# Kernel tuning notes

Hardware: AMD Instinct MI355X
Metric: run time of the kernel (lower is better)

## Reference

```python
import jax, jax.numpy as jnp
import numpy as np

DEGREE = 3
S_PNTS = 8          # sampling_points along polynomial
NUM_POINTS = 2      # deformable offsets per sampling point
S_SCALE = 0.077
SPATIAL = [(80, 80), (40, 40), (20, 20), (10, 10)]  # (h, w) per level
STARTS = [0, 6400, 8000, 8400]


def _lambdas():
    lam = jnp.linspace(0.0, 1.0, S_PNTS, dtype=jnp.float32)
    return jnp.stack([lam ** i for i in range(DEGREE, -1, -1)], 1)  # (S, degree+1)


def grid_sample_bilinear(img, grid):
    """torch F.grid_sample(mode=bilinear, padding_mode=zeros, align_corners=False).
    img: (B, C, H, W); grid: (B, Q, S, 2) with (x, y) in [-1, 1]. Returns (B, Q, S, C)."""
    B, C, H, W = img.shape
    gx = (grid[..., 0] + 1.0) * 0.5 * W - 0.5
    gy = (grid[..., 1] + 1.0) * 0.5 * H - 0.5
    x0 = jnp.floor(gx); y0 = jnp.floor(gy)
    x1 = x0 + 1.0;      y1 = y0 + 1.0
    wx1 = gx - x0; wx0 = 1.0 - wx1
    wy1 = gy - y0; wy0 = 1.0 - wy1
    flat = img.transpose(0, 2, 3, 1).reshape(B, H * W, C)  # (B, HW, C)
    Q, S = grid.shape[1], grid.shape[2]

    def fetch(xi, yi):
        valid = (xi >= 0) & (xi <= W - 1) & (yi >= 0) & (yi <= H - 1)
        xc = jnp.clip(xi, 0, W - 1).astype(jnp.int32)
        yc = jnp.clip(yi, 0, H - 1).astype(jnp.int32)
        idx = (yc * W + xc).reshape(B, Q * S, 1)
        vals = jnp.take_along_axis(flat, idx, axis=1).reshape(B, Q, S, C)
        return vals * valid[..., None].astype(img.dtype)

    out = (wy0 * wx0)[..., None] * fetch(x0, y0) \
        + (wy0 * wx1)[..., None] * fetch(x1, y0) \
        + (wy1 * wx0)[..., None] * fetch(x0, y1) \
        + (wy1 * wx1)[..., None] * fetch(x1, y1)
    return out  # (B, Q, S, C)


def setup_inputs() -> dict:
    key = jax.random.key(0)
    ks = jax.random.split(key, 6)
    B, Q, C = 8, 500, 256
    ref_polys = jax.random.uniform(ks[0], (B, Q, 2 * (DEGREE + 1)), dtype=jnp.float32)
    ref_levels = jax.random.randint(ks[1], (B, Q), 0, len(SPATIAL), dtype=jnp.int32)
    memory = jax.random.normal(ks[2], (B, 8500, C), dtype=jnp.float32)
    W1 = jax.random.normal(ks[3], (C, C), dtype=jnp.float32) * (1.0 / np.sqrt(C))
    b1 = jnp.zeros((C,), jnp.float32)
    W2 = jax.random.normal(ks[4], (C, 2 * NUM_POINTS), dtype=jnp.float32) * (1.0 / np.sqrt(C))
    b2 = jnp.zeros((2 * NUM_POINTS,), jnp.float32)
    return {"ref_polys": ref_polys, "ref_levels": ref_levels, "memory": memory,
            "W1": W1, "b1": b1, "W2": W2, "b2": b2}


def reference(ref_polys, ref_levels, memory, W1, b1, W2, b2):
    B, Q, _ = ref_polys.shape
    C = memory.shape[-1]
    lambdas = _lambdas()  # (S, degree+1)
    # polynomial evaluation: (B,Q,2,deg+1) @ (deg+1,S) -> (B,Q,S,2), mapped to [-1,1]
    rp = jax.lax.stop_gradient(ref_polys).reshape(B, Q, 2, DEGREE + 1)
    sampling_pts = 2.0 * (jnp.einsum('bqcd,sd->bqsc', rp, lambdas) - 0.5)  # (B,Q,S,2)
    # per-level bilinear sampling; memory slices reshaped to (B,C,h,w)
    sampled = []
    for (h, w), st in zip(SPATIAL, STARTS):
        lvl = memory[:, st:st + h * w, :].transpose(0, 2, 1).reshape(B, C, h, w)
        sampled.append(grid_sample_bilinear(lvl, sampling_pts))
    sampled = jnp.stack(sampled, 1)  # (B, L, Q, S, C)
    # gather the level assigned to each query
    idx = jnp.broadcast_to(ref_levels[:, None, :, None, None].astype(jnp.int32),
                           (B, 1, Q, S_PNTS, C))
    emb = jnp.take_along_axis(sampled, idx, axis=1)[:, 0]  # (B, Q, S, C)
    # 2-layer tanh MLP offset head
    h = jnp.tanh(emb @ W1 + b1)
    off = h @ W2 + b2  # (B, Q, S, 2*NUM_POINTS)
    off = S_SCALE * jnp.tanh(off.reshape(B, Q, S_PNTS, NUM_POINTS, 2))
    ref_points = off + sampling_pts[:, :, :, None, :]  # (B,Q,S,NP,2)
    return ref_points.reshape(B, Q, S_PNTS * NUM_POINTS, 2)
```

## Files before the change

kernel.cpp:

```cpp
#include <hip/hip_runtime.h>
#include <math.h>

#define S_PNTS 8
#define NUM_POINTS 2
#define NB 8
#define NQ 500
#define NC 256
#define S_SCALE 0.077f
#define QPB 8
#define ROWS (QPB * S_PNTS)
#define APAD 264

typedef __bf16 bf16x8 __attribute__((ext_vector_type(8)));
typedef __bf16 bf16x4 __attribute__((ext_vector_type(4)));
typedef float  f32x4  __attribute__((ext_vector_type(4)));

__device__ __forceinline__ float fast_tanh(float x) {
    float xc = fminf(fmaxf(x, -14.0f), 14.0f);
    float t  = __builtin_amdgcn_exp2f(xc * 2.88539008178f);
    return 1.0f - 2.0f * __builtin_amdgcn_rcpf(t + 1.0f);
}

__global__ __launch_bounds__(256) void prep_w1(const float* __restrict__ W1,
                                               __bf16* __restrict__ W1t) {
    __shared__ float tile[16][17];
    const int n0 = blockIdx.x * 16, k0 = blockIdx.y * 16;
    const int tx = threadIdx.x & 15, ty = threadIdx.x >> 4;
    tile[ty][tx] = W1[(k0 + ty) * NC + n0 + tx];
    __syncthreads();
    W1t[(n0 + ty) * NC + k0 + tx] = (__bf16)tile[tx][ty];
}

__global__ __launch_bounds__(256) void decoder_kernel(
    const float* __restrict__ ref_polys,
    const int*   __restrict__ ref_levels,
    const float* __restrict__ memory,
    const __bf16* __restrict__ W1t,
    const float* __restrict__ b1,
    const float* __restrict__ W2,
    const float* __restrict__ b2,
    float*       __restrict__ out)
{
    const int tid = threadIdx.x;

    __shared__ __bf16 emb_lds[ROWS * APAD];
    __shared__ float  w2t[4 * 260];
    __shared__ float  b1_lds[NC];
    __shared__ int4   p_idx[ROWS];
    __shared__ float4 p_w[ROWS];
    __shared__ float2 spts_lds[ROWS];

    if (tid < ROWS) {
        const int r = tid, s = r & 7;
        const int qg = blockIdx.x * QPB + (r >> 3);
        const int b  = qg / NQ;
        const int lvl = ref_levels[qg];
        const int W  = 80 >> lvl;
        const int st = (lvl >= 1) * 6400 + (lvl >= 2) * 1600 + (lvl >= 3) * 400;
        const float* rp = ref_polys + (size_t)qg * 8;
        float lam = (float)s * (1.0f / 7.0f);
        float sx = 2.0f * ((((rp[0] * lam + rp[1]) * lam + rp[2]) * lam + rp[3]) - 0.5f);
        float sy = 2.0f * ((((rp[4] * lam + rp[5]) * lam + rp[6]) * lam + rp[7]) - 0.5f);
        spts_lds[r] = make_float2(sx, sy);
        float gx = (sx + 1.0f) * 0.5f * (float)W - 0.5f;
        float gy = (sy + 1.0f) * 0.5f * (float)W - 0.5f;
        float x0f = floorf(gx), y0f = floorf(gy);
        int   x0 = (int)x0f,    y0 = (int)y0f;
        float wx1 = gx - x0f, wx0 = 1.0f - wx1;
        float wy1 = gy - y0f, wy0 = 1.0f - wy1;
        float xv0 = (x0 >= 0 && x0 < W) ? 1.0f : 0.0f;
        float xv1 = (x0 + 1 >= 0 && x0 + 1 < W) ? 1.0f : 0.0f;
        float yv0 = (y0 >= 0 && y0 < W) ? 1.0f : 0.0f;
        float yv1 = (y0 + 1 >= 0 && y0 + 1 < W) ? 1.0f : 0.0f;
        int xc0 = min(max(x0, 0), W - 1),     xc1 = min(max(x0 + 1, 0), W - 1);
        int yc0 = min(max(y0, 0), W - 1),     yc1 = min(max(y0 + 1, 0), W - 1);
        int base = b * 8500 + st;
        p_idx[r] = make_int4(base + yc0 * W + xc0, base + yc0 * W + xc1,
                             base + yc1 * W + xc0, base + yc1 * W + xc1);
        p_w[r] = make_float4(wy0 * wx0 * yv0 * xv0, wy0 * wx1 * yv0 * xv1,
                             wy1 * wx0 * yv1 * xv0, wy1 * wx1 * yv1 * xv1);
    }
    #pragma unroll
    for (int i = tid; i < NC * 4; i += 256) {
        int k = i >> 2, j = i & 3;
        w2t[j * 260 + k] = W2[i];
    }
    b1_lds[tid] = b1[tid];
    __syncthreads();

    {
        const int c4  = tid & 63;
        const int rg0 = tid >> 6;
        const float4* m4 = (const float4*)memory;
        #pragma unroll
        for (int i = 0; i < 16; ++i) {
            int r = i * 4 + rg0;
            int4   id = p_idx[r];
            float4 wv = p_w[r];
            float4 v00 = m4[(size_t)id.x * 64 + c4];
            float4 v01 = m4[(size_t)id.y * 64 + c4];
            float4 v10 = m4[(size_t)id.z * 64 + c4];
            float4 v11 = m4[(size_t)id.w * 64 + c4];
            bf16x4 e;
            e[0] = (__bf16)(wv.x * v00.x + wv.y * v01.x + wv.z * v10.x + wv.w * v11.x);
            e[1] = (__bf16)(wv.x * v00.y + wv.y * v01.y + wv.z * v10.y + wv.w * v11.y);
            e[2] = (__bf16)(wv.x * v00.z + wv.y * v01.z + wv.z * v10.z + wv.w * v11.z);
            e[3] = (__bf16)(wv.x * v00.w + wv.y * v01.w + wv.z * v10.w + wv.w * v11.w);
            *(bf16x4*)&emb_lds[r * APAD + c4 * 4] = e;
        }
    }
    __syncthreads();

    const int w    = tid >> 6;
    const int l    = tid & 63;
    const int lrow = l & 15;
    const int quad = l >> 4;

    f32x4 acc[4][4] = {};
    #pragma unroll
    for (int ks = 0; ks < 8; ++ks) {
        bf16x8 a[4];
        #pragma unroll
        for (int mt = 0; mt < 4; ++mt)
            a[mt] = *(const bf16x8*)&emb_lds[(mt * 16 + lrow) * APAD + ks * 32 + quad * 8];
        #pragma unroll
        for (int nt = 0; nt < 4; ++nt) {
            const int n = w * 64 + nt * 16 + lrow;
            bf16x8 bf = *(const bf16x8*)&W1t[n * NC + ks * 32 + quad * 8];
            #pragma unroll
            for (int mt = 0; mt < 4; ++mt)
                acc[mt][nt] = __builtin_amdgcn_mfma_f32_16x16x32_bf16(a[mt], bf, acc[mt][nt], 0, 0, 0);
        }
    }
    __syncthreads();

    #pragma unroll
    for (int mt = 0; mt < 4; ++mt) {
        #pragma unroll
        for (int nt = 0; nt < 4; ++nt) {
            const int n = w * 64 + nt * 16 + lrow;
            const float bias = b1_lds[n];
            #pragma unroll
            for (int rg = 0; rg < 4; ++rg) {
                const int row = mt * 16 + quad * 4 + rg;
                emb_lds[row * APAD + n] = (__bf16)fast_tanh(acc[mt][nt][rg] + bias);
            }
        }
    }
    __syncthreads();

    {
        const int r = tid >> 2;
        const int j = tid & 3;
        float sum = b2[j];
        #pragma unroll
        for (int i = 0; i < 32; ++i) {
            const int k = i * 8;
            bf16x8 hv = *(const bf16x8*)&emb_lds[r * APAD + k];
            f32x4 wa = *(const f32x4*)&w2t[j * 260 + k];
            f32x4 wb = *(const f32x4*)&w2t[j * 260 + k + 4];
            sum += (float)hv[0] * wa[0] + (float)hv[1] * wa[1]
                 + (float)hv[2] * wa[2] + (float)hv[3] * wa[3]
                 + (float)hv[4] * wb[0] + (float)hv[5] * wb[1]
                 + (float)hv[6] * wb[2] + (float)hv[7] * wb[3];
        }
        float o = S_SCALE * fast_tanh(sum);
        const int s  = r & 7;
        const int qg = blockIdx.x * QPB + (r >> 3);
        const int coord = j & 1;
        float sp = (coord == 0) ? spts_lds[r].x : spts_lds[r].y;
        out[(size_t)qg * 32 + s * 4 + j] = o + sp;
    }
}

extern "C" void kernel_launch(void* const* d_in, const int* in_sizes, int n_in,
                              void* d_out, int out_size, void* d_ws, size_t ws_size,
                              hipStream_t stream) {
    const float* ref_polys  = (const float*)d_in[0];
    const int*   ref_levels = (const int*)d_in[1];
    const float* memory     = (const float*)d_in[2];
    const float* W1         = (const float*)d_in[3];
    const float* b1         = (const float*)d_in[4];
    const float* W2         = (const float*)d_in[5];
    const float* b2         = (const float*)d_in[6];
    float* out = (float*)d_out;

    __bf16* W1t = (__bf16*)d_ws;

    prep_w1<<<dim3(16, 16), dim3(256), 0, stream>>>(W1, W1t);
    decoder_kernel<<<dim3(NB * NQ / QPB), dim3(256), 0, stream>>>(
        ref_polys, ref_levels, memory, W1t, b1, W2, b2, out);
}
```

Baseline: 126.5 us.

## Double decoder block size to 512 threads and split work across more waves

```diff
diff --git a/kernel.cpp b/kernel.cpp
--- a/kernel.cpp
+++ b/kernel.cpp
@@ -10,6 +10,7 @@
 #define QPB 8
 #define ROWS (QPB * S_PNTS)
 #define APAD 264
+#define BLK 512
 
 typedef __bf16 bf16x8 __attribute__((ext_vector_type(8)));
 typedef __bf16 bf16x4 __attribute__((ext_vector_type(4)));
@@ -31,7 +32,7 @@
     W1t[(n0 + ty) * NC + k0 + tx] = (__bf16)tile[tx][ty];
 }
 
-__global__ __launch_bounds__(256) void decoder_kernel(
+__global__ __launch_bounds__(BLK) void decoder_kernel(
     const float* __restrict__ ref_polys,
     const int*   __restrict__ ref_levels,
     const float* __restrict__ memory,
@@ -81,11 +82,11 @@
                              wy1 * wx0 * yv1 * xv0, wy1 * wx1 * yv1 * xv1);
     }
     #pragma unroll
-    for (int i = tid; i < NC * 4; i += 256) {
+    for (int i = tid; i < NC * 4; i += BLK) {
         int k = i >> 2, j = i & 3;
         w2t[j * 260 + k] = W2[i];
     }
-    b1_lds[tid] = b1[tid];
+    if (tid < NC) b1_lds[tid] = b1[tid];
     __syncthreads();
 
     {
@@ -93,8 +94,8 @@
         const int rg0 = tid >> 6;
         const float4* m4 = (const float4*)memory;
         #pragma unroll
-        for (int i = 0; i < 16; ++i) {
-            int r = i * 4 + rg0;
+        for (int i = 0; i < 8; ++i) {
+            int r = i * 8 + rg0;
             int4   id = p_idx[r];
             float4 wv = p_w[r];
             float4 v00 = m4[(size_t)id.x * 64 + c4];
@@ -112,37 +113,39 @@
     __syncthreads();
 
     const int w    = tid >> 6;
+    const int ns   = w & 3;
+    const int mh   = w >> 2;
     const int l    = tid & 63;
     const int lrow = l & 15;
     const int quad = l >> 4;
 
-    f32x4 acc[4][4] = {};
+    f32x4 acc[2][4] = {};
     #pragma unroll
     for (int ks = 0; ks < 8; ++ks) {
-        bf16x8 a[4];
-        #pragma unroll
-        for (int mt = 0; mt < 4; ++mt)
-            a[mt] = *(const bf16x8*)&emb_lds[(mt * 16 + lrow) * APAD + ks * 32 + quad * 8];
+        bf16x8 a[2];
+        #pragma unroll
+        for (int mt = 0; mt < 2; ++mt)
+            a[mt] = *(const bf16x8*)&emb_lds[(mh * 32 + mt * 16 + lrow) * APAD + ks * 32 + quad * 8];
         #pragma unroll
         for (int nt = 0; nt < 4; ++nt) {
-            const int n = w * 64 + nt * 16 + lrow;
+            const int n = ns * 64 + nt * 16 + lrow;
             bf16x8 bf = *(const bf16x8*)&W1t[n * NC + ks * 32 + quad * 8];
             #pragma unroll
-            for (int mt = 0; mt < 4; ++mt)
+            for (int mt = 0; mt < 2; ++mt)
                 acc[mt][nt] = __builtin_amdgcn_mfma_f32_16x16x32_bf16(a[mt], bf, acc[mt][nt], 0, 0, 0);
         }
     }
     __syncthreads();
 
     #pragma unroll
-    for (int mt = 0; mt < 4; ++mt) {
+    for (int mt = 0; mt < 2; ++mt) {
         #pragma unroll
         for (int nt = 0; nt < 4; ++nt) {
-            const int n = w * 64 + nt * 16 + lrow;
+            const int n = ns * 64 + nt * 16 + lrow;
             const float bias = b1_lds[n];
             #pragma unroll
             for (int rg = 0; rg < 4; ++rg) {
-                const int row = mt * 16 + quad * 4 + rg;
+                const int row = mh * 32 + mt * 16 + quad * 4 + rg;
                 emb_lds[row * APAD + n] = (__bf16)fast_tanh(acc[mt][nt][rg] + bias);
             }
         }
@@ -150,12 +153,14 @@
     __syncthreads();
 
     {
-        const int r = tid >> 2;
-        const int j = tid & 3;
-        float sum = b2[j];
-        #pragma unroll
-        for (int i = 0; i < 32; ++i) {
-            const int k = i * 8;
+        const int r    = tid >> 3;
+        const int j    = (tid >> 1) & 3;
+        const int half = tid & 1;
+        float sum = 0.0f;
+        const int kbase = half * 128;
+        #pragma unroll
+        for (int i = 0; i < 16; ++i) {
+            const int k = kbase + i * 8;
             bf16x8 hv = *(const bf16x8*)&emb_lds[r * APAD + k];
             f32x4 wa = *(const f32x4*)&w2t[j * 260 + k];
             f32x4 wb = *(const f32x4*)&w2t[j * 260 + k + 4];
@@ -164,12 +169,15 @@
                  + (float)hv[4] * wb[0] + (float)hv[5] * wb[1]
                  + (float)hv[6] * wb[2] + (float)hv[7] * wb[3];
         }
-        float o = S_SCALE * fast_tanh(sum);
-        const int s  = r & 7;
-        const int qg = blockIdx.x * QPB + (r >> 3);
-        const int coord = j & 1;
-        float sp = (coord == 0) ? spts_lds[r].x : spts_lds[r].y;
-        out[(size_t)qg * 32 + s * 4 + j] = o + sp;
+        sum += __shfl_xor(sum, 1);
+        if (half == 0) {
+            float o = S_SCALE * fast_tanh(sum + b2[j]);
+            const int s  = r & 7;
+            const int qg = blockIdx.x * QPB + (r >> 3);
+            const int coord = j & 1;
+            float sp = (coord == 0) ? spts_lds[r].x : spts_lds[r].y;
+            out[(size_t)qg * 32 + s * 4 + j] = o + sp;
+        }
     }
 }
 
@@ -188,6 +196,6 @@
     __bf16* W1t = (__bf16*)d_ws;
 
     prep_w1<<<dim3(16, 16), dim3(256), 0, stream>>>(W1, W1t);
-    decoder_kernel<<<dim3(NB * NQ / QPB), dim3(256), 0, stream>>>(
+    decoder_kernel<<<dim3(NB * NQ / QPB), dim3(BLK), 0, stream>>>(
         ref_polys, ref_levels, memory, W1t, b1, W2, b2, out);
 }
```

Result: slower. 129.3 us (+2.2%).
